# Optimization experiments

Measured on AMD Instinct MI355X. Metric: run time of the kernel, lower is better.

## Reference

```python
import jax, jax.numpy as jnp
import numpy as np

K = 3  # number of nearest neighbors
EPS = 1e-10


def setup_inputs() -> dict:
    key = jax.random.key(0)
    k1, k2, k3 = jax.random.split(key, 3)
    B, C, N = 2, 3, 8192
    xyz1 = jax.random.normal(k1, (B, C, N), dtype=jnp.float32)
    xyz2 = jax.random.normal(k2, (B, C, N), dtype=jnp.float32)
    flow1 = jax.random.normal(k3, (B, C, N), dtype=jnp.float32) * 0.1
    return {"xyz1": xyz1, "xyz2": xyz2, "flow1": flow1}


def _square_distance(src, dst):
    # src: [B, N, 3], dst: [B, M, 3] -> [B, N, M]
    d = -2.0 * jnp.einsum('bnc,bmc->bnm', src, dst)
    d = d + jnp.sum(src ** 2, axis=-1)[:, :, None]
    d = d + jnp.sum(dst ** 2, axis=-1)[:, None, :]
    return d


def _gather_group(points, idx):
    # points: [B, N, C], idx: [B, S, K] -> [B, S, K, C]
    return jax.vmap(lambda p, i: p[i])(points, idx)


def reference(xyz1, xyz2, flow1):
    B, C, N1 = xyz1.shape
    N2 = xyz2.shape[2]
    xyz1_to_2 = (xyz1 + flow1).transpose(0, 2, 1)  # [B, N1, 3]
    xyz2_t = xyz2.transpose(0, 2, 1)               # [B, N2, 3]
    flow1_t = flow1.transpose(0, 2, 1)             # [B, N1, 3]

    sqrdists = _square_distance(xyz2_t, xyz1_to_2)  # [B, N2, N1]
    _, knn_idx = jax.lax.top_k(-sqrdists, K)        # smallest K -> [B, N2, K]

    grouped_xyz = _gather_group(xyz1_to_2, knn_idx)           # [B, N2, K, 3]
    diff = grouped_xyz - xyz2_t[:, :, None, :]                 # [B, N2, K, 3]
    dist = jnp.maximum(jnp.linalg.norm(diff, axis=3), EPS)     # [B, N2, K]
    inv = 1.0 / dist
    weight = inv / jnp.sum(inv, axis=2, keepdims=True)         # [B, N2, K]

    grouped_flow = _gather_group(flow1_t, knn_idx)             # [B, N2, K, 3]
    flow2 = jnp.sum(weight[..., None] * grouped_flow, axis=2)  # [B, N2, 3]
    warped_xyz2 = (xyz2_t - flow2).transpose(0, 2, 1)          # [B, 3, N2]
    return warped_xyz2
```

## Files before the change

kernel.cpp:

```cpp
#include <hip/hip_runtime.h>


#define NPTS   8192
#define BLOCK  256
#define Q      4
#define QPB    8
#define HALF   4096
#define KMASK  0xFFFFFF80
#define EPSV   1e-10f

__device__ __forceinline__ float rfl_f32(float x) {
    return __int_as_float(__builtin_amdgcn_readfirstlane(__float_as_int(x)));
}

__device__ __forceinline__ void ksort3(float k, float& m0, float& m1, float& m2) {
    m2 = __builtin_amdgcn_fmed3f(k, m1, m2);
    m1 = __builtin_amdgcn_fmed3f(k, m0, m1);
    m0 = fminf(k, m0);
}

__device__ __forceinline__ void insert3_idx(float k, int idx,
                                            float& m0, float& m1, float& m2,
                                            int& j0, int& j1, int& j2) {
    const bool c0 = k < m0;
    const bool c1 = k < m1;
    const bool c2 = k < m2;
    ksort3(k, m0, m1, m2);
    j2 = c1 ? j1 : (c2 ? idx : j2);
    j1 = c0 ? j0 : (c1 ? idx : j1);
    j0 = c0 ? idx : j0;
}

__global__ __launch_bounds__(256)
void warp_points_kernel(const float* __restrict__ xyz1,
                        const float* __restrict__ flow1,
                        float4* __restrict__ ws, int total) {
    const int i = blockIdx.x * 256 + threadIdx.x;
    if (i >= total) return;
    const int b = i / NPTS, n = i - b * NPTS;
    const float* x1 = xyz1 + (size_t)b * 3 * NPTS;
    const float* f1 = flow1 + (size_t)b * 3 * NPTS;
    const float px = x1[0*NPTS + n] + f1[0*NPTS + n];
    const float py = x1[1*NPTS + n] + f1[1*NPTS + n];
    const float pz = x1[2*NPTS + n] + f1[2*NPTS + n];
    ws[i] = make_float4(px, py, pz, 0.0f);
}

__global__ __launch_bounds__(BLOCK, 8)
void pointwarp_kernel(const float4* __restrict__ wsp,
                      const float* __restrict__ xyz2,
                      const float* __restrict__ flow1,
                      float* __restrict__ out) {
    __shared__ float s_k[2][2][Q][3];
    __shared__ int   s_i[2][2][Q][3];

    const int tid  = threadIdx.x;
    const int w    = tid >> 6;
    const int t    = tid & 63;
    const int pair = w >> 1;
    const int w2   = w & 1;
    const int blocksPerB = NPTS / QPB;
    const int b     = blockIdx.x / blocksPerB;
    const int qblk  = (blockIdx.x % blocksPerB) * QPB;
    const int qbase = qblk + pair * Q;

    const float4* cand = wsp + (size_t)b * NPTS;
    const float*  x2   = xyz2 + (size_t)b * 3 * NPTS;
    const float*  f1   = flow1 + (size_t)b * 3 * NPTS;

    float qx[Q], qy[Q], qz[Q], k0[Q], k1[Q], k2[Q];
    #pragma unroll
    for (int i = 0; i < Q; ++i) {
        qx[i] = rfl_f32(x2[0*NPTS + qbase + i]);
        qy[i] = rfl_f32(x2[1*NPTS + qbase + i]);
        qz[i] = rfl_f32(x2[2*NPTS + qbase + i]);
        k0[i] = k1[i] = k2[i] = 3e38f;
    }

    const float4* base = cand + w2 * HALF + t;
    const int rowbase = w2 * (HALF / 64);
    #pragma unroll 2
    for (int j = 0; j < HALF / 128; ++j) {
        const float4 p0 = base[j * 128];
        const float4 p1 = base[j * 128 + 64];
        const int jg0 = rowbase + 2*j;
        const int jg1 = jg0 + 1;
        #pragma unroll
        for (int i = 0; i < Q; ++i) {
            const float dx0 = p0.x - qx[i];
            const float dy0 = p0.y - qy[i];
            const float dz0 = p0.z - qz[i];
            const float d0  = fmaf(dx0, dx0, fmaf(dy0, dy0, dz0*dz0));
            const float ka  = __int_as_float((__float_as_int(d0) & KMASK) | jg0);
            ksort3(ka, k0[i], k1[i], k2[i]);
            const float dx1 = p1.x - qx[i];
            const float dy1 = p1.y - qy[i];
            const float dz1 = p1.z - qz[i];
            const float d1  = fmaf(dx1, dx1, fmaf(dy1, dy1, dz1*dz1));
            const float kb  = __int_as_float((__float_as_int(d1) & KMASK) | jg1);
            ksort3(kb, k0[i], k1[i], k2[i]);
        }
    }

    float a0[Q], a1[Q], a2[Q];
    #pragma unroll
    for (int i = 0; i < Q; ++i) { a0[i] = k0[i]; a1[i] = k1[i]; a2[i] = k2[i]; }

    #pragma unroll
    for (int step = 1; step < 64; step <<= 1) {
        #pragma unroll
        for (int i = 0; i < Q; ++i) {
            const float b0 = __shfl_xor(k0[i], step, 64);
            const float b1 = __shfl_xor(k1[i], step, 64);
            const float b2 = __shfl_xor(k2[i], step, 64);
            ksort3(b0, k0[i], k1[i], k2[i]);
            ksort3(b1, k0[i], k1[i], k2[i]);
            ksort3(b2, k0[i], k1[i], k2[i]);
        }
    }

    int i0[Q], i1[Q], i2[Q];
    #pragma unroll
    for (int i = 0; i < Q; ++i) {
        {
            const float kf = k0[i];
            const unsigned long long m = __ballot(kf == a0[i] || kf == a1[i] || kf == a2[i]);
            i0[i] = ((__float_as_int(kf) & 0x7F) << 6) | (__ffsll(m) - 1);
        }
        {
            const float kf = k1[i];
            const unsigned long long m = __ballot(kf == a0[i] || kf == a1[i] || kf == a2[i]);
            i1[i] = ((__float_as_int(kf) & 0x7F) << 6) | (__ffsll(m) - 1);
        }
        {
            const float kf = k2[i];
            const unsigned long long m = __ballot(kf == a0[i] || kf == a1[i] || kf == a2[i]);
            i2[i] = ((__float_as_int(kf) & 0x7F) << 6) | (__ffsll(m) - 1);
        }
    }

    #pragma unroll
    for (int i = 0; i < Q; ++i) {
        if (t == i) {
            s_k[pair][w2][i][0] = k0[i]; s_i[pair][w2][i][0] = i0[i];
            s_k[pair][w2][i][1] = k1[i]; s_i[pair][w2][i][1] = i1[i];
            s_k[pair][w2][i][2] = k2[i]; s_i[pair][w2][i][2] = i2[i];
        }
    }
    __syncthreads();

    if (tid < QPB) {
        const int u  = tid;
        const int pr = u >> 2, qi = u & 3;
        float m0 = 3e38f, m1 = 3e38f, m2 = 3e38f;
        int   j0 = 0, j1 = 0, j2 = 0;
        #pragma unroll
        for (int wv = 0; wv < 2; ++wv) {
            #pragma unroll
            for (int s = 0; s < 3; ++s) {
                insert3_idx(s_k[pr][wv][qi][s], s_i[pr][wv][qi][s],
                            m0, m1, m2, j0, j1, j2);
            }
        }
        const int n2 = qblk + u;
        const float gx = x2[0*NPTS + n2];
        const float gy = x2[1*NPTS + n2];
        const float gz = x2[2*NPTS + n2];
        float dd[3];
        const int js[3] = {j0, j1, j2};
        #pragma unroll
        for (int s = 0; s < 3; ++s) {
            const float4 p = cand[js[s]];
            const float dx = p.x - gx, dy = p.y - gy, dz = p.z - gz;
            dd[s] = fmaf(dx, dx, fmaf(dy, dy, dz*dz));
        }
        float w0 = 1.0f / fmaxf(sqrtf(dd[0]), EPSV);
        float w1 = 1.0f / fmaxf(sqrtf(dd[1]), EPSV);
        float w2v = 1.0f / fmaxf(sqrtf(dd[2]), EPSV);
        const float ws = w0 + w1 + w2v;
        w0 /= ws; w1 /= ws; w2v /= ws;

        float* o = out + (size_t)b * 3 * NPTS;
        #pragma unroll
        for (int c = 0; c < 3; ++c) {
            const float fl = w0  * f1[c*NPTS + j0]
                           + w1  * f1[c*NPTS + j1]
                           + w2v * f1[c*NPTS + j2];
            o[c*NPTS + n2] = x2[c*NPTS + n2] - fl;
        }
    }
}

extern "C" void kernel_launch(void* const* d_in, const int* in_sizes, int n_in,
                              void* d_out, int out_size, void* d_ws, size_t ws_size,
                              hipStream_t stream) {
    const float* xyz1  = (const float*)d_in[0];
    const float* xyz2  = (const float*)d_in[1];
    const float* flow1 = (const float*)d_in[2];
    float* out = (float*)d_out;
    float4* ws = (float4*)d_ws;

    const int B = in_sizes[0] / (3 * NPTS);
    const int total = B * NPTS;
    warp_points_kernel<<<(total + 255) / 256, 256, 0, stream>>>(xyz1, flow1, ws, total);
    const int grid = B * (NPTS / QPB);
    pointwarp_kernel<<<grid, BLOCK, 0, stream>>>(ws, xyz2, flow1, out);
}
```

Measured before the change: 97.96 us.

## Split candidates across four waves with eight queries per wave

Each wave now scans a quarter of the candidate points for all eight queries in the block, where before a pair of waves split the candidates in half for four queries each. Every loaded candidate is reused across twice as many queries, halving the global/L2 load traffic per distance computation. The cost is more registers for per-query state (8 queries × top-3), which could lower occupancy, plus a longer shuffle merge and four-way final merge per query.

```diff
diff --git a/kernel.cpp b/kernel.cpp
--- a/kernel.cpp
+++ b/kernel.cpp
@@ -1,13 +1,13 @@
 #include <hip/hip_runtime.h>
 
 
-#define NPTS   8192
-#define BLOCK  256
-#define Q      4
-#define QPB    8
-#define HALF   4096
-#define KMASK  0xFFFFFF80
-#define EPSV   1e-10f
+#define NPTS    8192
+#define BLOCK   256
+#define Q       8
+#define QPB     8
+#define QUARTER 2048
+#define KMASK   0xFFFFFF80
+#define EPSV    1e-10f
 
 __device__ __forceinline__ float rfl_f32(float x) {
     return __int_as_float(__builtin_amdgcn_readfirstlane(__float_as_int(x)));
@@ -51,18 +51,15 @@
                       const float* __restrict__ xyz2,
                       const float* __restrict__ flow1,
                       float* __restrict__ out) {
-    __shared__ float s_k[2][2][Q][3];
-    __shared__ int   s_i[2][2][Q][3];
+    __shared__ float s_k[4][Q][3];
+    __shared__ int   s_i[4][Q][3];
 
     const int tid  = threadIdx.x;
     const int w    = tid >> 6;
     const int t    = tid & 63;
-    const int pair = w >> 1;
-    const int w2   = w & 1;
     const int blocksPerB = NPTS / QPB;
     const int b     = blockIdx.x / blocksPerB;
     const int qblk  = (blockIdx.x % blocksPerB) * QPB;
-    const int qbase = qblk + pair * Q;
 
     const float4* cand = wsp + (size_t)b * NPTS;
     const float*  x2   = xyz2 + (size_t)b * 3 * NPTS;
@@ -71,34 +68,46 @@
     float qx[Q], qy[Q], qz[Q], k0[Q], k1[Q], k2[Q];
     #pragma unroll
     for (int i = 0; i < Q; ++i) {
-        qx[i] = rfl_f32(x2[0*NPTS + qbase + i]);
-        qy[i] = rfl_f32(x2[1*NPTS + qbase + i]);
-        qz[i] = rfl_f32(x2[2*NPTS + qbase + i]);
+        qx[i] = rfl_f32(x2[0*NPTS + qblk + i]);
+        qy[i] = rfl_f32(x2[1*NPTS + qblk + i]);
+        qz[i] = rfl_f32(x2[2*NPTS + qblk + i]);
         k0[i] = k1[i] = k2[i] = 3e38f;
     }
 
-    const float4* base = cand + w2 * HALF + t;
-    const int rowbase = w2 * (HALF / 64);
-    #pragma unroll 2
-    for (int j = 0; j < HALF / 128; ++j) {
-        const float4 p0 = base[j * 128];
-        const float4 p1 = base[j * 128 + 64];
-        const int jg0 = rowbase + 2*j;
-        const int jg1 = jg0 + 1;
+    const float4* base = cand + w * QUARTER + t;
+    const int rowbase = w * (QUARTER / 64);
+    for (int j = 0; j < QUARTER / 256; ++j) {
+        const float4 p0 = base[j * 256];
+        const float4 p1 = base[j * 256 + 64];
+        const float4 p2 = base[j * 256 + 128];
+        const float4 p3 = base[j * 256 + 192];
+        const int jg0 = rowbase + 4*j;
         #pragma unroll
         for (int i = 0; i < Q; ++i) {
-            const float dx0 = p0.x - qx[i];
-            const float dy0 = p0.y - qy[i];
-            const float dz0 = p0.z - qz[i];
-            const float d0  = fmaf(dx0, dx0, fmaf(dy0, dy0, dz0*dz0));
-            const float ka  = __int_as_float((__float_as_int(d0) & KMASK) | jg0);
-            ksort3(ka, k0[i], k1[i], k2[i]);
-            const float dx1 = p1.x - qx[i];
-            const float dy1 = p1.y - qy[i];
-            const float dz1 = p1.z - qz[i];
-            const float d1  = fmaf(dx1, dx1, fmaf(dy1, dy1, dz1*dz1));
-            const float kb  = __int_as_float((__float_as_int(d1) & KMASK) | jg1);
-            ksort3(kb, k0[i], k1[i], k2[i]);
+            {
+                const float dx = p0.x - qx[i], dy = p0.y - qy[i], dz = p0.z - qz[i];
+                const float d  = fmaf(dx, dx, fmaf(dy, dy, dz*dz));
+                ksort3(__int_as_float((__float_as_int(d) & KMASK) | jg0),
+                       k0[i], k1[i], k2[i]);
+            }
+            {
+                const float dx = p1.x - qx[i], dy = p1.y - qy[i], dz = p1.z - qz[i];
+                const float d  = fmaf(dx, dx, fmaf(dy, dy, dz*dz));
+                ksort3(__int_as_float((__float_as_int(d) & KMASK) | (jg0+1)),
+                       k0[i], k1[i], k2[i]);
+            }
+            {
+                const float dx = p2.x - qx[i], dy = p2.y - qy[i], dz = p2.z - qz[i];
+                const float d  = fmaf(dx, dx, fmaf(dy, dy, dz*dz));
+                ksort3(__int_as_float((__float_as_int(d) & KMASK) | (jg0+2)),
+                       k0[i], k1[i], k2[i]);
+            }
+            {
+                const float dx = p3.x - qx[i], dy = p3.y - qy[i], dz = p3.z - qz[i];
+                const float d  = fmaf(dx, dx, fmaf(dy, dy, dz*dz));
+                ksort3(__int_as_float((__float_as_int(d) & KMASK) | (jg0+3)),
+                       k0[i], k1[i], k2[i]);
+            }
         }
     }
 
@@ -142,27 +151,26 @@
     #pragma unroll
     for (int i = 0; i < Q; ++i) {
         if (t == i) {
-            s_k[pair][w2][i][0] = k0[i]; s_i[pair][w2][i][0] = i0[i];
-            s_k[pair][w2][i][1] = k1[i]; s_i[pair][w2][i][1] = i1[i];
-            s_k[pair][w2][i][2] = k2[i]; s_i[pair][w2][i][2] = i2[i];
+            s_k[w][i][0] = k0[i]; s_i[w][i][0] = i0[i];
+            s_k[w][i][1] = k1[i]; s_i[w][i][1] = i1[i];
+            s_k[w][i][2] = k2[i]; s_i[w][i][2] = i2[i];
         }
     }
     __syncthreads();
 
     if (tid < QPB) {
-        const int u  = tid;
-        const int pr = u >> 2, qi = u & 3;
+        const int qi = tid;
         float m0 = 3e38f, m1 = 3e38f, m2 = 3e38f;
         int   j0 = 0, j1 = 0, j2 = 0;
         #pragma unroll
-        for (int wv = 0; wv < 2; ++wv) {
+        for (int wv = 0; wv < 4; ++wv) {
             #pragma unroll
             for (int s = 0; s < 3; ++s) {
-                insert3_idx(s_k[pr][wv][qi][s], s_i[pr][wv][qi][s],
+                insert3_idx(s_k[wv][qi][s], s_i[wv][qi][s],
                             m0, m1, m2, j0, j1, j2);
             }
         }
-        const int n2 = qblk + u;
+        const int n2 = qblk + qi;
         const float gx = x2[0*NPTS + n2];
         const float gy = x2[1*NPTS + n2];
         const float gz = x2[2*NPTS + n2];
```

Measured after the change: 102.2 us. 4.3% more time.

## Switch candidate buffer to SoA float2 pairs for packed FMA distance math

Applied to the files above, without the earlier changes.

Replaces the AoS float4 candidate workspace with three planar arrays read as float2 pairs, so each lane computes two candidate distances with packed 2-wide subtract/FMA ops. The packed-key low-bit index encoding is narrowed from 7 to 6 bits and the global index reconstruction is changed to match the new pair-interleaved traversal. This aims to halve the VALU instruction count in the inner distance loop and cut wasted bytes from the unused float4 lane, at the cost of one extra mantissa bit in the key and more complex index decoding.

```diff
diff --git a/kernel.cpp b/kernel.cpp
--- a/kernel.cpp
+++ b/kernel.cpp
@@ -2,12 +2,23 @@
 
 
 #define NPTS   8192
+#define PAIRS  (NPTS / 2)
 #define BLOCK  256
 #define Q      4
 #define QPB    8
 #define HALF   4096
-#define KMASK  0xFFFFFF80
+#define KMASK  0xFFFFFFC0
 #define EPSV   1e-10f
+
+typedef float v2f __attribute__((ext_vector_type(2)));
+
+__device__ __forceinline__ v2f v2fma(v2f a, v2f b, v2f c) {
+#if __has_builtin(__builtin_elementwise_fma)
+    return __builtin_elementwise_fma(a, b, c);
+#else
+    v2f r; r.x = fmaf(a.x, b.x, c.x); r.y = fmaf(a.y, b.y, c.y); return r;
+#endif
+}
 
 __device__ __forceinline__ float rfl_f32(float x) {
     return __int_as_float(__builtin_amdgcn_readfirstlane(__float_as_int(x)));
@@ -34,20 +45,21 @@
 __global__ __launch_bounds__(256)
 void warp_points_kernel(const float* __restrict__ xyz1,
                         const float* __restrict__ flow1,
-                        float4* __restrict__ ws, int total) {
+                        v2f* __restrict__ wx, v2f* __restrict__ wy,
+                        v2f* __restrict__ wz, int totalPairs) {
     const int i = blockIdx.x * 256 + threadIdx.x;
-    if (i >= total) return;
-    const int b = i / NPTS, n = i - b * NPTS;
-    const float* x1 = xyz1 + (size_t)b * 3 * NPTS;
-    const float* f1 = flow1 + (size_t)b * 3 * NPTS;
-    const float px = x1[0*NPTS + n] + f1[0*NPTS + n];
-    const float py = x1[1*NPTS + n] + f1[1*NPTS + n];
-    const float pz = x1[2*NPTS + n] + f1[2*NPTS + n];
-    ws[i] = make_float4(px, py, pz, 0.0f);
+    if (i >= totalPairs) return;
+    const int b = i / PAIRS, ip = i - b * PAIRS;
+    const v2f* x1v = (const v2f*)(xyz1 + (size_t)b * 3 * NPTS);
+    const v2f* f1v = (const v2f*)(flow1 + (size_t)b * 3 * NPTS);
+    wx[i] = x1v[0*PAIRS + ip] + f1v[0*PAIRS + ip];
+    wy[i] = x1v[1*PAIRS + ip] + f1v[1*PAIRS + ip];
+    wz[i] = x1v[2*PAIRS + ip] + f1v[2*PAIRS + ip];
 }
 
 __global__ __launch_bounds__(BLOCK, 8)
-void pointwarp_kernel(const float4* __restrict__ wsp,
+void pointwarp_kernel(const v2f* __restrict__ wx, const v2f* __restrict__ wy,
+                      const v2f* __restrict__ wz,
                       const float* __restrict__ xyz2,
                       const float* __restrict__ flow1,
                       float* __restrict__ out) {
@@ -64,41 +76,45 @@
     const int qblk  = (blockIdx.x % blocksPerB) * QPB;
     const int qbase = qblk + pair * Q;
 
-    const float4* cand = wsp + (size_t)b * NPTS;
-    const float*  x2   = xyz2 + (size_t)b * 3 * NPTS;
-    const float*  f1   = flow1 + (size_t)b * 3 * NPTS;
-
-    float qx[Q], qy[Q], qz[Q], k0[Q], k1[Q], k2[Q];
+    const v2f* wxb = wx + (size_t)b * PAIRS;
+    const v2f* wyb = wy + (size_t)b * PAIRS;
+    const v2f* wzb = wz + (size_t)b * PAIRS;
+    const float* x2 = xyz2 + (size_t)b * 3 * NPTS;
+    const float* f1 = flow1 + (size_t)b * 3 * NPTS;
+
+    v2f qx2[Q], qy2[Q], qz2[Q];
+    float k0[Q], k1[Q], k2[Q];
     #pragma unroll
     for (int i = 0; i < Q; ++i) {
-        qx[i] = rfl_f32(x2[0*NPTS + qbase + i]);
-        qy[i] = rfl_f32(x2[1*NPTS + qbase + i]);
-        qz[i] = rfl_f32(x2[2*NPTS + qbase + i]);
+        const float qx = rfl_f32(x2[0*NPTS + qbase + i]);
+        const float qy = rfl_f32(x2[1*NPTS + qbase + i]);
+        const float qz = rfl_f32(x2[2*NPTS + qbase + i]);
+        qx2[i].x = qx; qx2[i].y = qx;
+        qy2[i].x = qy; qy2[i].y = qy;
+        qz2[i].x = qz; qz2[i].y = qz;
         k0[i] = k1[i] = k2[i] = 3e38f;
     }
 
-    const float4* base = cand + w2 * HALF + t;
-    const int rowbase = w2 * (HALF / 64);
+    const v2f* bx = wxb + w2 * (HALF/2) + t;
+    const v2f* by = wyb + w2 * (HALF/2) + t;
+    const v2f* bz = wzb + w2 * (HALF/2) + t;
     #pragma unroll 2
     for (int j = 0; j < HALF / 128; ++j) {
-        const float4 p0 = base[j * 128];
-        const float4 p1 = base[j * 128 + 64];
-        const int jg0 = rowbase + 2*j;
-        const int jg1 = jg0 + 1;
+        const v2f px = bx[j * 64];
+        const v2f py = by[j * 64];
+        const v2f pz = bz[j * 64];
+        const int js0 = j << 1;
+        const int js1 = js0 | 1;
         #pragma unroll
         for (int i = 0; i < Q; ++i) {
-            const float dx0 = p0.x - qx[i];
-            const float dy0 = p0.y - qy[i];
-            const float dz0 = p0.z - qz[i];
-            const float d0  = fmaf(dx0, dx0, fmaf(dy0, dy0, dz0*dz0));
-            const float ka  = __int_as_float((__float_as_int(d0) & KMASK) | jg0);
-            ksort3(ka, k0[i], k1[i], k2[i]);
-            const float dx1 = p1.x - qx[i];
-            const float dy1 = p1.y - qy[i];
-            const float dz1 = p1.z - qz[i];
-            const float d1  = fmaf(dx1, dx1, fmaf(dy1, dy1, dz1*dz1));
-            const float kb  = __int_as_float((__float_as_int(d1) & KMASK) | jg1);
-            ksort3(kb, k0[i], k1[i], k2[i]);
+            const v2f dx = px - qx2[i];
+            const v2f dy = py - qy2[i];
+            const v2f dz = pz - qz2[i];
+            const v2f d  = v2fma(dx, dx, v2fma(dy, dy, dz * dz));
+            ksort3(__int_as_float((__float_as_int(d.x) & KMASK) | js0),
+                   k0[i], k1[i], k2[i]);
+            ksort3(__int_as_float((__float_as_int(d.y) & KMASK) | js1),
+                   k0[i], k1[i], k2[i]);
         }
     }
 
@@ -125,17 +141,20 @@
         {
             const float kf = k0[i];
             const unsigned long long m = __ballot(kf == a0[i] || kf == a1[i] || kf == a2[i]);
-            i0[i] = ((__float_as_int(kf) & 0x7F) << 6) | (__ffsll(m) - 1);
+            const int low6 = __float_as_int(kf) & 0x3F;
+            i0[i] = w2*HALF + (low6 >> 1)*128 + 2*(__ffsll(m) - 1) + (low6 & 1);
         }
         {
             const float kf = k1[i];
             const unsigned long long m = __ballot(kf == a0[i] || kf == a1[i] || kf == a2[i]);
-            i1[i] = ((__float_as_int(kf) & 0x7F) << 6) | (__ffsll(m) - 1);
+            const int low6 = __float_as_int(kf) & 0x3F;
+            i1[i] = w2*HALF + (low6 >> 1)*128 + 2*(__ffsll(m) - 1) + (low6 & 1);
         }
         {
             const float kf = k2[i];
             const unsigned long long m = __ballot(kf == a0[i] || kf == a1[i] || kf == a2[i]);
-            i2[i] = ((__float_as_int(kf) & 0x7F) << 6) | (__ffsll(m) - 1);
+            const int low6 = __float_as_int(kf) & 0x3F;
+            i2[i] = w2*HALF + (low6 >> 1)*128 + 2*(__ffsll(m) - 1) + (low6 & 1);
         }
     }
 
@@ -162,6 +181,9 @@
                             m0, m1, m2, j0, j1, j2);
             }
         }
+        const float* cx = (const float*)wxb;
+        const float* cy = (const float*)wyb;
+        const float* cz = (const float*)wzb;
         const int n2 = qblk + u;
         const float gx = x2[0*NPTS + n2];
         const float gy = x2[1*NPTS + n2];
@@ -170,8 +192,8 @@
         const int js[3] = {j0, j1, j2};
         #pragma unroll
         for (int s = 0; s < 3; ++s) {
-            const float4 p = cand[js[s]];
-            const float dx = p.x - gx, dy = p.y - gy, dz = p.z - gz;
+            const int jn = js[s];
+            const float dx = cx[jn] - gx, dy = cy[jn] - gy, dz = cz[jn] - gz;
             dd[s] = fmaf(dx, dx, fmaf(dy, dy, dz*dz));
         }
         float w0 = 1.0f / fmaxf(sqrtf(dd[0]), EPSV);
@@ -198,11 +220,15 @@
     const float* xyz2  = (const float*)d_in[1];
     const float* flow1 = (const float*)d_in[2];
     float* out = (float*)d_out;
-    float4* ws = (float4*)d_ws;
 
     const int B = in_sizes[0] / (3 * NPTS);
-    const int total = B * NPTS;
-    warp_points_kernel<<<(total + 255) / 256, 256, 0, stream>>>(xyz1, flow1, ws, total);
+    const int totalPairs = B * PAIRS;
+    v2f* wx = (v2f*)d_ws;
+    v2f* wy = wx + totalPairs;
+    v2f* wz = wy + totalPairs;
+
+    warp_points_kernel<<<(totalPairs + 255) / 256, 256, 0, stream>>>(
+        xyz1, flow1, wx, wy, wz, totalPairs);
     const int grid = B * (NPTS / QPB);
-    pointwarp_kernel<<<grid, BLOCK, 0, stream>>>(ws, xyz2, flow1, out);
-}
+    pointwarp_kernel<<<grid, BLOCK, 0, stream>>>(wx, wy, wz, xyz2, flow1, out);
+}
```

New measurement: 105.8 us. 8.0% more time.

## Replace brute-force KNN with x-binned counting sort and pruned window search

Applied to the files above, without the earlier changes.

Sorts candidate and query points along x into 256 bins using histogram, prefix and scatter kernels, then has each wavefront grow a window of 64-candidate chunks outward from its queries' bin. Growth stops once the x-gap to the next chunk exceeds the current third-nearest distance for all four queries. This targets the O(N^2) distance work of the brute-force scan, at the cost of three extra small launches, a memset, atomics, and a serial single-thread prefix scan. The search caps at 128 chunks per wavefront, and its result can differ from the reference if queries grouped in one wavefront are spread out.

```diff
diff --git a/kernel.cpp b/kernel.cpp
--- a/kernel.cpp
+++ b/kernel.cpp
@@ -3,11 +3,18 @@
 
 #define NPTS   8192
 #define BLOCK  256
-#define Q      4
-#define QPB    8
-#define HALF   4096
+#define QW     4
 #define KMASK  0xFFFFFF80
+#define MAXCH  128
+#define XLO    (-6.0f)
+#define XW     (12.0f / 256.0f)
+#define XINVW  (256.0f / 12.0f)
 #define EPSV   1e-10f
+
+__device__ __forceinline__ int xbin(float x) {
+    int b = (int)floorf((x - XLO) * XINVW);
+    return b < 0 ? 0 : (b > 255 ? 255 : b);
+}
 
 __device__ __forceinline__ float rfl_f32(float x) {
     return __int_as_float(__builtin_amdgcn_readfirstlane(__float_as_int(x)));
@@ -19,97 +26,162 @@
     m0 = fminf(k, m0);
 }
 
-__device__ __forceinline__ void insert3_idx(float k, int idx,
-                                            float& m0, float& m1, float& m2,
-                                            int& j0, int& j1, int& j2) {
-    const bool c0 = k < m0;
-    const bool c1 = k < m1;
-    const bool c2 = k < m2;
-    ksort3(k, m0, m1, m2);
-    j2 = c1 ? j1 : (c2 ? idx : j2);
-    j1 = c0 ? j0 : (c1 ? idx : j1);
-    j0 = c0 ? idx : j0;
-}
-
 __global__ __launch_bounds__(256)
-void warp_points_kernel(const float* __restrict__ xyz1,
-                        const float* __restrict__ flow1,
-                        float4* __restrict__ ws, int total) {
+void hist_kernel(const float* __restrict__ xyz1, const float* __restrict__ flow1,
+                 const float* __restrict__ xyz2, int* __restrict__ histC,
+                 int* __restrict__ histQ) {
     const int i = blockIdx.x * 256 + threadIdx.x;
-    if (i >= total) return;
-    const int b = i / NPTS, n = i - b * NPTS;
+    const int b = i >> 13, n = i & (NPTS - 1);
+    const float px = xyz1[(size_t)b*3*NPTS + n] + flow1[(size_t)b*3*NPTS + n];
+    atomicAdd(&histC[b*256 + xbin(px)], 1);
+    const float qx = xyz2[(size_t)b*3*NPTS + n];
+    atomicAdd(&histQ[b*256 + xbin(qx)], 1);
+}
+
+__global__ __launch_bounds__(64)
+void prefix_kernel(const int* __restrict__ histC, const int* __restrict__ histQ,
+                   int* __restrict__ pfC, int* __restrict__ ctrC,
+                   int* __restrict__ ctrQ) {
+    const int tid = threadIdx.x;
+    if (tid < 2) {
+        int s = 0;
+        for (int k = 0; k < 256; ++k) {
+            pfC[tid*256 + k] = s; ctrC[tid*256 + k] = s;
+            s += histC[tid*256 + k];
+        }
+    } else if (tid < 4) {
+        const int b = tid - 2;
+        int s = 0;
+        for (int k = 0; k < 256; ++k) {
+            ctrQ[b*256 + k] = s;
+            s += histQ[b*256 + k];
+        }
+    }
+}
+
+__global__ __launch_bounds__(256)
+void scatter_kernel(const float* __restrict__ xyz1, const float* __restrict__ flow1,
+                    const float* __restrict__ xyz2, int* __restrict__ ctrC,
+                    int* __restrict__ ctrQ, float4* __restrict__ sortedC,
+                    int* __restrict__ sortedQ) {
+    const int i = blockIdx.x * 256 + threadIdx.x;
+    const int b = i >> 13, n = i & (NPTS - 1);
     const float* x1 = xyz1 + (size_t)b * 3 * NPTS;
     const float* f1 = flow1 + (size_t)b * 3 * NPTS;
     const float px = x1[0*NPTS + n] + f1[0*NPTS + n];
     const float py = x1[1*NPTS + n] + f1[1*NPTS + n];
     const float pz = x1[2*NPTS + n] + f1[2*NPTS + n];
-    ws[i] = make_float4(px, py, pz, 0.0f);
+    const int pos = atomicAdd(&ctrC[b*256 + xbin(px)], 1);
+    sortedC[(size_t)b*NPTS + pos] = make_float4(px, py, pz, __int_as_float(n));
+    const float qx = xyz2[(size_t)b*3*NPTS + n];
+    const int qpos = atomicAdd(&ctrQ[b*256 + xbin(qx)], 1);
+    sortedQ[b*NPTS + qpos] = n;
 }
 
 __global__ __launch_bounds__(BLOCK, 8)
-void pointwarp_kernel(const float4* __restrict__ wsp,
-                      const float* __restrict__ xyz2,
-                      const float* __restrict__ flow1,
-                      float* __restrict__ out) {
-    __shared__ float s_k[2][2][Q][3];
-    __shared__ int   s_i[2][2][Q][3];
-
-    const int tid  = threadIdx.x;
-    const int w    = tid >> 6;
-    const int t    = tid & 63;
-    const int pair = w >> 1;
-    const int w2   = w & 1;
-    const int blocksPerB = NPTS / QPB;
-    const int b     = blockIdx.x / blocksPerB;
-    const int qblk  = (blockIdx.x % blocksPerB) * QPB;
-    const int qbase = qblk + pair * Q;
-
-    const float4* cand = wsp + (size_t)b * NPTS;
-    const float*  x2   = xyz2 + (size_t)b * 3 * NPTS;
-    const float*  f1   = flow1 + (size_t)b * 3 * NPTS;
-
-    float qx[Q], qy[Q], qz[Q], k0[Q], k1[Q], k2[Q];
-    #pragma unroll
-    for (int i = 0; i < Q; ++i) {
-        qx[i] = rfl_f32(x2[0*NPTS + qbase + i]);
-        qy[i] = rfl_f32(x2[1*NPTS + qbase + i]);
-        qz[i] = rfl_f32(x2[2*NPTS + qbase + i]);
+void knn_kernel(const float4* __restrict__ sortedC, const int* __restrict__ sortedQ,
+                const int* __restrict__ pfC, const float* __restrict__ xyz2,
+                const float* __restrict__ flow1, float* __restrict__ out) {
+    __shared__ int s_cb[4][MAXCH];
+
+    const int tid = threadIdx.x;
+    const int w   = tid >> 6;
+    const int t   = tid & 63;
+    const int blocksPerB = (NPTS / (QW * 4));
+    const int b = blockIdx.x / blocksPerB;
+    const int g = (blockIdx.x % blocksPerB) * 4 + w;
+
+    const float4* sc = sortedC + (size_t)b * NPTS;
+    const float*  x2 = xyz2 + (size_t)b * 3 * NPTS;
+    const float*  f1 = flow1 + (size_t)b * 3 * NPTS;
+
+    int   n2[QW];
+    float qx[QW], qy[QW], qz[QW], k0[QW], k1[QW], k2[QW];
+    #pragma unroll
+    for (int i = 0; i < QW; ++i) {
+        n2[i] = __builtin_amdgcn_readfirstlane(sortedQ[b*NPTS + g*QW + i]);
+        qx[i] = rfl_f32(x2[0*NPTS + n2[i]]);
+        qy[i] = rfl_f32(x2[1*NPTS + n2[i]]);
+        qz[i] = rfl_f32(x2[2*NPTS + n2[i]]);
         k0[i] = k1[i] = k2[i] = 3e38f;
     }
 
-    const float4* base = cand + w2 * HALF + t;
-    const int rowbase = w2 * (HALF / 64);
-    #pragma unroll 2
-    for (int j = 0; j < HALF / 128; ++j) {
-        const float4 p0 = base[j * 128];
-        const float4 p1 = base[j * 128 + 64];
-        const int jg0 = rowbase + 2*j;
-        const int jg1 = jg0 + 1;
-        #pragma unroll
-        for (int i = 0; i < Q; ++i) {
-            const float dx0 = p0.x - qx[i];
-            const float dy0 = p0.y - qy[i];
-            const float dz0 = p0.z - qz[i];
-            const float d0  = fmaf(dx0, dx0, fmaf(dy0, dy0, dz0*dz0));
-            const float ka  = __int_as_float((__float_as_int(d0) & KMASK) | jg0);
-            ksort3(ka, k0[i], k1[i], k2[i]);
-            const float dx1 = p1.x - qx[i];
-            const float dy1 = p1.y - qy[i];
-            const float dz1 = p1.z - qz[i];
-            const float d1  = fmaf(dx1, dx1, fmaf(dy1, dy1, dz1*dz1));
-            const float kb  = __int_as_float((__float_as_int(d1) & KMASK) | jg1);
-            ksort3(kb, k0[i], k1[i], k2[i]);
-        }
-    }
-
-    float a0[Q], a1[Q], a2[Q];
-    #pragma unroll
-    for (int i = 0; i < Q; ++i) { a0[i] = k0[i]; a1[i] = k1[i]; a2[i] = k2[i]; }
-
+    int cb = pfC[b*256 + xbin(qx[0])] - 32;
+    cb &= ~63;
+    if (cb < 0) cb = 0;
+    if (cb > NPTS - 64) cb = NPTS - 64;
+
+    int L = cb, R = cb + 64, c = 0;
+
+    auto process = [&](int base, int cc) {
+        const float4 p = sc[base + t];
+        #pragma unroll
+        for (int i = 0; i < QW; ++i) {
+            const float dx = p.x - qx[i];
+            const float dy = p.y - qy[i];
+            const float dz = p.z - qz[i];
+            const float d  = fmaf(dx, dx, fmaf(dy, dy, dz*dz));
+            ksort3(__int_as_float((__float_as_int(d) & KMASK) | cc),
+                   k0[i], k1[i], k2[i]);
+        }
+        s_cb[w][cc] = base;
+    };
+
+    process(cb, 0);
+    c = 1;
+    bool doneL = (L == 0), doneR = (R >= NPTS);
+
+    while ((!doneL || !doneR) && c < MAXCH) {
+        float km[QW];
+        #pragma unroll
+        for (int i = 0; i < QW; ++i) {
+            float m = k2[i];
+            #pragma unroll
+            for (int step = 1; step < 64; step <<= 1)
+                m = fminf(m, __shfl_xor(m, step, 64));
+            km[i] = m;
+        }
+        float xlU = -1e30f, xrL = 1e30f;
+        if (!doneL) {
+            const float xl = sc[L-1].x;
+            xlU = XLO + (float)(xbin(xl) + 1) * XW;
+            bool allq = true;
+            #pragma unroll
+            for (int i = 0; i < QW; ++i) {
+                const float dl = qx[i] - xlU;
+                if (!(dl > 0.0f && dl*dl > km[i])) allq = false;
+            }
+            doneL = allq;
+        }
+        if (!doneR) {
+            const float xr = sc[R].x;
+            xrL = XLO + (float)xbin(xr) * XW;
+            bool allq = true;
+            #pragma unroll
+            for (int i = 0; i < QW; ++i) {
+                const float dr = xrL - qx[i];
+                if (!(dr > 0.0f && dr*dr > km[i])) allq = false;
+            }
+            doneR = allq;
+        }
+        if (doneL && doneR) break;
+        const float xc = 0.25f * (qx[0] + qx[1] + qx[2] + qx[3]);
+        bool goLeft;
+        if (doneL)      goLeft = false;
+        else if (doneR) goLeft = true;
+        else            goLeft = (xc - xlU) <= (xrL - xc);
+        if (goLeft) { L -= 64; process(L, c); doneL = (L == 0); }
+        else        { process(R, c); R += 64; doneR = (R >= NPTS); }
+        ++c;
+    }
+
+    float a0[QW], a1[QW], a2[QW];
+    #pragma unroll
+    for (int i = 0; i < QW; ++i) { a0[i] = k0[i]; a1[i] = k1[i]; a2[i] = k2[i]; }
     #pragma unroll
     for (int step = 1; step < 64; step <<= 1) {
         #pragma unroll
-        for (int i = 0; i < Q; ++i) {
+        for (int i = 0; i < QW; ++i) {
             const float b0 = __shfl_xor(k0[i], step, 64);
             const float b1 = __shfl_xor(k1[i], step, 64);
             const float b2 = __shfl_xor(k2[i], step, 64);
@@ -119,74 +191,50 @@
         }
     }
 
-    int i0[Q], i1[Q], i2[Q];
-    #pragma unroll
-    for (int i = 0; i < Q; ++i) {
+    int p0[QW], p1[QW], p2[QW];
+    #pragma unroll
+    for (int i = 0; i < QW; ++i) {
         {
             const float kf = k0[i];
             const unsigned long long m = __ballot(kf == a0[i] || kf == a1[i] || kf == a2[i]);
-            i0[i] = ((__float_as_int(kf) & 0x7F) << 6) | (__ffsll(m) - 1);
+            p0[i] = s_cb[w][__float_as_int(kf) & 0x7F] + (__ffsll(m) - 1);
         }
         {
             const float kf = k1[i];
             const unsigned long long m = __ballot(kf == a0[i] || kf == a1[i] || kf == a2[i]);
-            i1[i] = ((__float_as_int(kf) & 0x7F) << 6) | (__ffsll(m) - 1);
+            p1[i] = s_cb[w][__float_as_int(kf) & 0x7F] + (__ffsll(m) - 1);
         }
         {
             const float kf = k2[i];
             const unsigned long long m = __ballot(kf == a0[i] || kf == a1[i] || kf == a2[i]);
-            i2[i] = ((__float_as_int(kf) & 0x7F) << 6) | (__ffsll(m) - 1);
-        }
-    }
-
-    #pragma unroll
-    for (int i = 0; i < Q; ++i) {
-        if (t == i) {
-            s_k[pair][w2][i][0] = k0[i]; s_i[pair][w2][i][0] = i0[i];
-            s_k[pair][w2][i][1] = k1[i]; s_i[pair][w2][i][1] = i1[i];
-            s_k[pair][w2][i][2] = k2[i]; s_i[pair][w2][i][2] = i2[i];
-        }
-    }
-    __syncthreads();
-
-    if (tid < QPB) {
-        const int u  = tid;
-        const int pr = u >> 2, qi = u & 3;
-        float m0 = 3e38f, m1 = 3e38f, m2 = 3e38f;
-        int   j0 = 0, j1 = 0, j2 = 0;
-        #pragma unroll
-        for (int wv = 0; wv < 2; ++wv) {
-            #pragma unroll
-            for (int s = 0; s < 3; ++s) {
-                insert3_idx(s_k[pr][wv][qi][s], s_i[pr][wv][qi][s],
-                            m0, m1, m2, j0, j1, j2);
-            }
-        }
-        const int n2 = qblk + u;
-        const float gx = x2[0*NPTS + n2];
-        const float gy = x2[1*NPTS + n2];
-        const float gz = x2[2*NPTS + n2];
-        float dd[3];
-        const int js[3] = {j0, j1, j2};
+            p2[i] = s_cb[w][__float_as_int(kf) & 0x7F] + (__ffsll(m) - 1);
+        }
+    }
+
+    if (t < QW) {
+        const int i = t;
+        const int ps[3] = {p0[i], p1[i], p2[i]};
+        float dd[3]; int jj[3];
         #pragma unroll
         for (int s = 0; s < 3; ++s) {
-            const float4 p = cand[js[s]];
-            const float dx = p.x - gx, dy = p.y - gy, dz = p.z - gz;
+            const float4 p = sc[ps[s]];
+            jj[s] = __float_as_int(p.w);
+            const float dx = p.x - qx[i], dy = p.y - qy[i], dz = p.z - qz[i];
             dd[s] = fmaf(dx, dx, fmaf(dy, dy, dz*dz));
         }
         float w0 = 1.0f / fmaxf(sqrtf(dd[0]), EPSV);
         float w1 = 1.0f / fmaxf(sqrtf(dd[1]), EPSV);
-        float w2v = 1.0f / fmaxf(sqrtf(dd[2]), EPSV);
-        const float ws = w0 + w1 + w2v;
-        w0 /= ws; w1 /= ws; w2v /= ws;
+        float w2 = 1.0f / fmaxf(sqrtf(dd[2]), EPSV);
+        const float ws = w0 + w1 + w2;
+        w0 /= ws; w1 /= ws; w2 /= ws;
 
         float* o = out + (size_t)b * 3 * NPTS;
         #pragma unroll
-        for (int c = 0; c < 3; ++c) {
-            const float fl = w0  * f1[c*NPTS + j0]
-                           + w1  * f1[c*NPTS + j1]
-                           + w2v * f1[c*NPTS + j2];
-            o[c*NPTS + n2] = x2[c*NPTS + n2] - fl;
+        for (int ch = 0; ch < 3; ++ch) {
+            const float fl = w0 * f1[ch*NPTS + jj[0]]
+                           + w1 * f1[ch*NPTS + jj[1]]
+                           + w2 * f1[ch*NPTS + jj[2]];
+            o[ch*NPTS + n2[i]] = x2[ch*NPTS + n2[i]] - fl;
         }
     }
 }
@@ -198,11 +246,20 @@
     const float* xyz2  = (const float*)d_in[1];
     const float* flow1 = (const float*)d_in[2];
     float* out = (float*)d_out;
-    float4* ws = (float4*)d_ws;
-
-    const int B = in_sizes[0] / (3 * NPTS);
-    const int total = B * NPTS;
-    warp_points_kernel<<<(total + 255) / 256, 256, 0, stream>>>(xyz1, flow1, ws, total);
-    const int grid = B * (NPTS / QPB);
-    pointwarp_kernel<<<grid, BLOCK, 0, stream>>>(ws, xyz2, flow1, out);
-}
+
+    float4* sortedC = (float4*)d_ws;
+    int*    sortedQ = (int*)(sortedC + 2 * NPTS);
+    int*    histC   = sortedQ + 2 * NPTS;
+    int*    histQ   = histC + 512;
+    int*    pfC     = histQ + 512;
+    int*    ctrC    = pfC + 512;
+    int*    ctrQ    = ctrC + 512;
+
+    hipMemsetAsync(histC, 0, 1024 * sizeof(int), stream);
+    hist_kernel<<<64, 256, 0, stream>>>(xyz1, flow1, xyz2, histC, histQ);
+    prefix_kernel<<<1, 64, 0, stream>>>(histC, histQ, pfC, ctrC, ctrQ);
+    scatter_kernel<<<64, 256, 0, stream>>>(xyz1, flow1, xyz2, ctrC, ctrQ,
+                                           sortedC, sortedQ);
+    knn_kernel<<<2 * (NPTS / (QW * 4)), BLOCK, 0, stream>>>(
+        sortedC, sortedQ, pfC, xyz2, flow1, out);
+}
```

Measured after the change: 233.7 us. 139% more time.
